# Optimization experiments

Measured on AMD Instinct MI355X. Metric: run time of the kernel, lower is better.

## Reference

```python
import jax, jax.numpy as jnp
import numpy as np

DEP_NUM, HEAD_NUM, BSZ, DIM, REL = 96, 96, 16, 512, 128


def setup_inputs() -> dict:
    key = jax.random.key(0)
    k1, k2, k3, k4 = jax.random.split(key, 4)
    outs = jax.random.normal(k1, (DEP_NUM, BSZ, DIM), dtype=jnp.float32)
    graph_state = jax.random.normal(k2, (HEAD_NUM, BSZ, DIM), dtype=jnp.float32)
    # nn.init.normal_(std=0.02) for both weights, zero biases
    Wt = 0.02 * jax.random.normal(k3, (DIM, 2 * DIM), dtype=jnp.float32)
    bt = jnp.zeros((DIM,), dtype=jnp.float32)
    Wp = 0.02 * jax.random.normal(k4, (REL, DIM), dtype=jnp.float32)
    bp = jnp.zeros((REL,), dtype=jnp.float32)
    return {"outs": outs, "graph_state": graph_state, "Wt": Wt, "bt": bt, "Wp": Wp, "bp": bp}


def reference(outs, graph_state, Wt, bt, Wp, bp):
    # outs: [dep, b, D], graph_state: [head, b, D]
    # Linear(cat(dep, head)) == dep @ Wt[:, :D].T + head @ Wt[:, D:].T + bt
    D = outs.shape[-1]
    dep_proj = jnp.einsum('dbi,ei->dbe', outs, Wt[:, :D])           # [dep, b, D]
    head_proj = jnp.einsum('hbi,ei->hbe', graph_state, Wt[:, D:])   # [head, b, D]
    # broadcast-sum to pairwise: [dep, b, head, D]
    h = jax.nn.relu(dep_proj[:, :, None, :] + jnp.swapaxes(head_proj, 0, 1)[None] + bt)
    # dropout: identity in eval mode
    scores = jnp.einsum('dbhe,re->dbhr', h, Wp) + bp                # [dep, b, head, REL]
    nil = jnp.zeros(scores.shape[:-1] + (1,), dtype=scores.dtype)
    scores = jnp.concatenate([nil, scores], axis=-1)                # [dep, b, head, REL+1]
    return jax.nn.log_softmax(scores, axis=-1)
```

## Files before the change

### kernel.cpp

```cpp
#include <hip/hip_runtime.h>
#include <hip/hip_bf16.h>
#include <math.h>

#define DEP   96
#define HEADS 96
#define BSZ   16
#define DIM   512
#define REL   128
#define RELP  129

typedef __attribute__((ext_vector_type(8))) short short8;
typedef __attribute__((ext_vector_type(4))) float floatx4;

__device__ __forceinline__ unsigned short f2bf(float x) {
    union { float f; unsigned int u; } c; c.f = x;
    unsigned int r = c.u + 0x7fffu + ((c.u >> 16) & 1u);
    return (unsigned short)(r >> 16);
}
__device__ __forceinline__ float bflo2f(unsigned int u) {
    union { unsigned int u; float f; } c; c.u = u << 16; return c.f;
}
__device__ __forceinline__ float bfhi2f(unsigned int u) {
    union { unsigned int u; float f; } c; c.u = u & 0xffff0000u; return c.f;
}

__global__ __launch_bounds__(256) void cvt_kernel(
    const float* __restrict__ Wt, const float* __restrict__ Wp,
    unsigned short* __restrict__ WtB, unsigned short* __restrict__ WpB)
{
    const int chunk = blockIdx.x * 256 + threadIdx.x;
    const float* src; unsigned short* dst; int c;
    if (chunk < 65536) { src = Wt; dst = WtB; c = chunk; }
    else               { src = Wp; dst = WpB; c = chunk - 65536; }
    float4 a = *(const float4*)(src + (size_t)c * 8);
    float4 b = *(const float4*)(src + (size_t)c * 8 + 4);
    uint4 o;
    o.x = (unsigned)f2bf(a.x) | ((unsigned)f2bf(a.y) << 16);
    o.y = (unsigned)f2bf(a.z) | ((unsigned)f2bf(a.w) << 16);
    o.z = (unsigned)f2bf(b.x) | ((unsigned)f2bf(b.y) << 16);
    o.w = (unsigned)f2bf(b.z) | ((unsigned)f2bf(b.w) << 16);
    *(uint4*)(dst + (size_t)c * 8) = o;
}

#define PSS 72

__global__ __launch_bounds__(256) void proj_kernel(
    const float* __restrict__ outs, const float* __restrict__ graph,
    const unsigned short* __restrict__ WtB, const float* __restrict__ bt,
    float* __restrict__ P1, unsigned short* __restrict__ P2B)
{
    const int z = blockIdx.z;
    const float* A = z ? graph : outs;
    const int off  = z ? DIM : 0;
    const int row0 = blockIdx.y * 64;
    const int col0 = blockIdx.x * 64;

    __shared__ unsigned short As[64 * PSS];
    __shared__ unsigned short Ws[64 * PSS];

    const int tid  = threadIdx.x;
    const int lane = tid & 63;
    const int wv   = tid >> 6;
    const int ln15 = lane & 15;
    const int quad = lane >> 4;

    floatx4 acc[4];
    #pragma unroll
    for (int nt = 0; nt < 4; ++nt) acc[nt] = (floatx4){0.f,0.f,0.f,0.f};

    for (int kt = 0; kt < DIM; kt += 64) {
        #pragma unroll
        for (int q = 0; q < 4; ++q) {
            const int slot = q*256 + tid;
            const int r  = slot >> 4;
            const int e4 = (slot & 15) * 4;
            float4 v = *(const float4*)(A + (size_t)(row0 + r) * DIM + kt + e4);
            ushort4 o;
            o.x = f2bf(v.x); o.y = f2bf(v.y); o.z = f2bf(v.z); o.w = f2bf(v.w);
            *(ushort4*)&As[r * PSS + e4] = o;
        }
        #pragma unroll
        for (int q = 0; q < 2; ++q) {
            const int slot = q*256 + tid;
            const int r  = slot >> 3;
            const int e8 = (slot & 7) * 8;
            *(uint4*)&Ws[r * PSS + e8] =
                *(const uint4*)(WtB + (size_t)(col0 + r) * (2*DIM) + off + kt + e8);
        }
        __syncthreads();
        #pragma unroll
        for (int ks = 0; ks < 64; ks += 32) {
            short8 af = *(const short8*)&As[(wv*16 + ln15) * PSS + ks + quad*8];
            #pragma unroll
            for (int nt = 0; nt < 4; ++nt) {
                short8 bf8 = *(const short8*)&Ws[(nt*16 + ln15) * PSS + ks + quad*8];
                acc[nt] = __builtin_amdgcn_mfma_f32_16x16x32_bf16(af, bf8, acc[nt], 0, 0, 0);
            }
        }
        __syncthreads();
    }

    #pragma unroll
    for (int nt = 0; nt < 4; ++nt) {
        #pragma unroll
        for (int reg = 0; reg < 4; ++reg) {
            const int m = row0 + wv*16 + quad*4 + reg;
            const int n = col0 + nt*16 + ln15;
            float v = acc[nt][reg];
            if (!z) P1[(size_t)m * DIM + n] = v + bt[n];
            else    P2B[(size_t)m * DIM + n] = f2bf(v);
        }
    }
}

#define HSS 72
#define WSS 72

__global__ __launch_bounds__(256, 4) void fused_kernel(
    const float* __restrict__ P1, const unsigned short* __restrict__ P2B,
    const unsigned short* __restrict__ WpB, const float* __restrict__ bp,
    float* __restrict__ out)
{
    const int db = blockIdx.x;
    const int b  = db & 15;

    __shared__ float          drow[DIM];
    __shared__ unsigned short hs[96 * HSS];
    __shared__ unsigned short ws[128 * WSS];
    __shared__ float          pmx[96][2];
    __shared__ float          pl [96][2];

    const int tid  = threadIdx.x;
    const int lane = tid & 63;
    const int wv   = tid >> 6;
    const int ln15 = lane & 15;
    const int quad = lane >> 4;
    const int mh   = wv & 1;
    const int nh   = wv >> 1;

    drow[tid]       = P1[(size_t)db * DIM + tid];
    drow[tid + 256] = P1[(size_t)db * DIM + tid + 256];
    __syncthreads();

    floatx4 acc[3][4];
    #pragma unroll
    for (int i = 0; i < 3; ++i)
        #pragma unroll
        for (int j = 0; j < 4; ++j) acc[i][j] = (floatx4){0.f,0.f,0.f,0.f};

    for (int kt = 0; kt < DIM; kt += 64) {
        #pragma unroll
        for (int q = 0; q < 3; ++q) {
            const int slot = q*256 + tid;
            const int h  = slot >> 3;
            const int e8 = (slot & 7) * 8;
            uint4 pv = *(const uint4*)(P2B + ((size_t)h * BSZ + b) * DIM + kt + e8);
            float4 d0 = *(const float4*)&drow[kt + e8];
            float4 d1 = *(const float4*)&drow[kt + e8 + 4];
            float s0 = fmaxf(bflo2f(pv.x) + d0.x, 0.f);
            float s1 = fmaxf(bfhi2f(pv.x) + d0.y, 0.f);
            float s2 = fmaxf(bflo2f(pv.y) + d0.z, 0.f);
            float s3 = fmaxf(bfhi2f(pv.y) + d0.w, 0.f);
            float s4 = fmaxf(bflo2f(pv.z) + d1.x, 0.f);
            float s5 = fmaxf(bfhi2f(pv.z) + d1.y, 0.f);
            float s6 = fmaxf(bflo2f(pv.w) + d1.z, 0.f);
            float s7 = fmaxf(bfhi2f(pv.w) + d1.w, 0.f);
            uint4 o;
            o.x = (unsigned)f2bf(s0) | ((unsigned)f2bf(s1) << 16);
            o.y = (unsigned)f2bf(s2) | ((unsigned)f2bf(s3) << 16);
            o.z = (unsigned)f2bf(s4) | ((unsigned)f2bf(s5) << 16);
            o.w = (unsigned)f2bf(s6) | ((unsigned)f2bf(s7) << 16);
            *(uint4*)&hs[h * HSS + e8] = o;
        }
        #pragma unroll
        for (int q = 0; q < 4; ++q) {
            const int slot = q*256 + tid;
            const int r = slot >> 3;
            const int g = (slot & 7) * 8;
            *(uint4*)&ws[r * WSS + g] =
                *(const uint4*)(WpB + (size_t)r * DIM + kt + g);
        }
        __syncthreads();

        #pragma unroll
        for (int ks = 0; ks < 64; ks += 32) {
            short8 af[3], bf8[4];
            #pragma unroll
            for (int mt = 0; mt < 3; ++mt)
                af[mt] = *(const short8*)&hs[(mh*48 + mt*16 + ln15) * HSS + ks + quad*8];
            #pragma unroll
            for (int nt = 0; nt < 4; ++nt)
                bf8[nt] = *(const short8*)&ws[(nh*64 + nt*16 + ln15) * WSS + ks + quad*8];
            #pragma unroll
            for (int nt = 0; nt < 4; ++nt)
                #pragma unroll
                for (int mt = 0; mt < 3; ++mt)
                    acc[mt][nt] = __builtin_amdgcn_mfma_f32_16x16x32_bf16(
                        af[mt], bf8[nt], acc[mt][nt], 0, 0, 0);
        }
        __syncthreads();
    }

    float bpv[4];
    #pragma unroll
    for (int nt = 0; nt < 4; ++nt) bpv[nt] = bp[nh*64 + nt*16 + ln15];

    #pragma unroll
    for (int mt = 0; mt < 3; ++mt) {
        #pragma unroll
        for (int reg = 0; reg < 4; ++reg) {
            const int m = mh*48 + mt*16 + quad*4 + reg;
            float s[4];
            float mx = -1e30f;
            #pragma unroll
            for (int nt = 0; nt < 4; ++nt) {
                s[nt] = acc[mt][nt][reg] + bpv[nt];
                mx = fmaxf(mx, s[nt]);
            }
            #pragma unroll
            for (int msk = 1; msk < 16; msk <<= 1) mx = fmaxf(mx, __shfl_xor(mx, msk));
            float l = 0.f;
            #pragma unroll
            for (int nt = 0; nt < 4; ++nt) l += __expf(s[nt] - mx);
            #pragma unroll
            for (int msk = 1; msk < 16; msk <<= 1) l += __shfl_xor(l, msk);
            if (ln15 == 0) { pmx[m][nh] = mx; pl[m][nh] = l; }
        }
    }
    __syncthreads();

    #pragma unroll
    for (int mt = 0; mt < 3; ++mt) {
        #pragma unroll
        for (int reg = 0; reg < 4; ++reg) {
            const int m = mh*48 + mt*16 + quad*4 + reg;
            const float mx0 = pmx[m][0], mx1 = pmx[m][1];
            const float l0  = pl[m][0],  l1  = pl[m][1];
            const float MX = fmaxf(fmaxf(mx0, mx1), 0.f);
            const float L  = l0 * __expf(mx0 - MX) + l1 * __expf(mx1 - MX)
                           + __expf(-MX);
            const float lse = MX + __logf(L);

            const size_t base = ((size_t)db * HEADS + m) * RELP;
            #pragma unroll
            for (int nt = 0; nt < 4; ++nt)
                out[base + 1 + nh*64 + nt*16 + ln15] = acc[mt][nt][reg] + bpv[nt] - lse;
            if (nh == 0 && ln15 == 0) out[base] = -lse;
        }
    }
}

extern "C" void kernel_launch(void* const* d_in, const int* in_sizes, int n_in,
                              void* d_out, int out_size, void* d_ws, size_t ws_size,
                              hipStream_t stream) {
    const float* outs  = (const float*)d_in[0];
    const float* graph = (const float*)d_in[1];
    const float* Wt    = (const float*)d_in[2];
    const float* bt    = (const float*)d_in[3];
    const float* Wp    = (const float*)d_in[4];
    const float* bp    = (const float*)d_in[5];
    float* out = (float*)d_out;

    float* P1           = (float*)d_ws;
    unsigned short* P2B = (unsigned short*)(P1 + 786432);
    unsigned short* WpB = P2B + 786432;
    unsigned short* WtB = WpB + 65536;

    cvt_kernel<<<288, 256, 0, stream>>>(Wt, Wp, WtB, WpB);
    proj_kernel<<<dim3(DIM/64, (DEP*BSZ)/64, 2), 256, 0, stream>>>(
        outs, graph, WtB, bt, P1, P2B);
    fused_kernel<<<DEP*BSZ, 256, 0, stream>>>(P1, P2B, WpB, bp, out);
}
```

Baseline: 161.0 us.

## Switch fused pairwise stage to fp16 with packed math and direct global MFMA operand loads

The head projection, the dep row and Wp now use fp16 instead of bf16. The relu(dep+head) combine is done with packed v_pk_add_f16/v_pk_max_f16 directly in registers. The shared-memory staging of the hidden tile and Wp, along with its barriers, is removed, so MFMA operands are loaded straight from global memory (relying on L1/L2 reuse) into f16 MFMAs. This drops LDS traffic, sync and scalar fp32 conversions. The risks are more global/L2 loads per wave, a lower occupancy hint (3 instead of 4 waves per SIMD), and fp16 range and precision in the add.

```diff
diff --git a/kernel.cpp b/kernel.cpp
--- a/kernel.cpp
+++ b/kernel.cpp
@@ -9,37 +9,53 @@
 #define REL   128
 #define RELP  129
 
-typedef __attribute__((ext_vector_type(8))) short short8;
-typedef __attribute__((ext_vector_type(4))) float floatx4;
+typedef __attribute__((ext_vector_type(8))) short     short8;
+typedef __attribute__((ext_vector_type(8))) _Float16  half8;
+typedef __attribute__((ext_vector_type(4))) float     floatx4;
 
 __device__ __forceinline__ unsigned short f2bf(float x) {
     union { float f; unsigned int u; } c; c.f = x;
     unsigned int r = c.u + 0x7fffu + ((c.u >> 16) & 1u);
     return (unsigned short)(r >> 16);
 }
-__device__ __forceinline__ float bflo2f(unsigned int u) {
-    union { unsigned int u; float f; } c; c.u = u << 16; return c.f;
-}
-__device__ __forceinline__ float bfhi2f(unsigned int u) {
-    union { unsigned int u; float f; } c; c.u = u & 0xffff0000u; return c.f;
+__device__ __forceinline__ unsigned short f2h(float x) {
+    union { _Float16 h; unsigned short u; } c;
+    c.h = (_Float16)x;
+    return c.u;
+}
+__device__ __forceinline__ unsigned pk_add_h2(unsigned a, unsigned b) {
+    unsigned r; asm("v_pk_add_f16 %0, %1, %2" : "=v"(r) : "v"(a), "v"(b)); return r;
+}
+__device__ __forceinline__ unsigned pk_max_h2(unsigned a, unsigned b) {
+    unsigned r; asm("v_pk_max_f16 %0, %1, %2" : "=v"(r) : "v"(a), "v"(b)); return r;
 }
 
 __global__ __launch_bounds__(256) void cvt_kernel(
     const float* __restrict__ Wt, const float* __restrict__ Wp,
-    unsigned short* __restrict__ WtB, unsigned short* __restrict__ WpB)
+    unsigned short* __restrict__ WtB, unsigned short* __restrict__ WpH)
 {
     const int chunk = blockIdx.x * 256 + threadIdx.x;
-    const float* src; unsigned short* dst; int c;
-    if (chunk < 65536) { src = Wt; dst = WtB; c = chunk; }
-    else               { src = Wp; dst = WpB; c = chunk - 65536; }
-    float4 a = *(const float4*)(src + (size_t)c * 8);
-    float4 b = *(const float4*)(src + (size_t)c * 8 + 4);
-    uint4 o;
-    o.x = (unsigned)f2bf(a.x) | ((unsigned)f2bf(a.y) << 16);
-    o.y = (unsigned)f2bf(a.z) | ((unsigned)f2bf(a.w) << 16);
-    o.z = (unsigned)f2bf(b.x) | ((unsigned)f2bf(b.y) << 16);
-    o.w = (unsigned)f2bf(b.z) | ((unsigned)f2bf(b.w) << 16);
-    *(uint4*)(dst + (size_t)c * 8) = o;
+    if (chunk < 65536) {
+        const int c = chunk;
+        float4 a = *(const float4*)(Wt + (size_t)c * 8);
+        float4 b = *(const float4*)(Wt + (size_t)c * 8 + 4);
+        uint4 o;
+        o.x = (unsigned)f2bf(a.x) | ((unsigned)f2bf(a.y) << 16);
+        o.y = (unsigned)f2bf(a.z) | ((unsigned)f2bf(a.w) << 16);
+        o.z = (unsigned)f2bf(b.x) | ((unsigned)f2bf(b.y) << 16);
+        o.w = (unsigned)f2bf(b.z) | ((unsigned)f2bf(b.w) << 16);
+        *(uint4*)(WtB + (size_t)c * 8) = o;
+    } else {
+        const int c = chunk - 65536;
+        float4 a = *(const float4*)(Wp + (size_t)c * 8);
+        float4 b = *(const float4*)(Wp + (size_t)c * 8 + 4);
+        uint4 o;
+        o.x = (unsigned)f2h(a.x) | ((unsigned)f2h(a.y) << 16);
+        o.y = (unsigned)f2h(a.z) | ((unsigned)f2h(a.w) << 16);
+        o.z = (unsigned)f2h(b.x) | ((unsigned)f2h(b.y) << 16);
+        o.w = (unsigned)f2h(b.z) | ((unsigned)f2h(b.w) << 16);
+        *(uint4*)(WpH + (size_t)c * 8) = o;
+    }
 }
 
 #define PSS 72
@@ -47,7 +63,7 @@
 __global__ __launch_bounds__(256) void proj_kernel(
     const float* __restrict__ outs, const float* __restrict__ graph,
     const unsigned short* __restrict__ WtB, const float* __restrict__ bt,
-    float* __restrict__ P1, unsigned short* __restrict__ P2B)
+    float* __restrict__ P1, unsigned short* __restrict__ P2H)
 {
     const int z = blockIdx.z;
     const float* A = z ? graph : outs;
@@ -108,27 +124,22 @@
             const int n = col0 + nt*16 + ln15;
             float v = acc[nt][reg];
             if (!z) P1[(size_t)m * DIM + n] = v + bt[n];
-            else    P2B[(size_t)m * DIM + n] = f2bf(v);
-        }
-    }
-}
-
-#define HSS 72
-#define WSS 72
-
-__global__ __launch_bounds__(256, 4) void fused_kernel(
-    const float* __restrict__ P1, const unsigned short* __restrict__ P2B,
-    const unsigned short* __restrict__ WpB, const float* __restrict__ bp,
+            else    P2H[(size_t)m * DIM + n] = f2h(v);
+        }
+    }
+}
+
+__global__ __launch_bounds__(256, 3) void fused_kernel(
+    const float* __restrict__ P1, const unsigned short* __restrict__ P2H,
+    const unsigned short* __restrict__ WpH, const float* __restrict__ bp,
     float* __restrict__ out)
 {
     const int db = blockIdx.x;
     const int b  = db & 15;
 
-    __shared__ float          drow[DIM];
-    __shared__ unsigned short hs[96 * HSS];
-    __shared__ unsigned short ws[128 * WSS];
-    __shared__ float          pmx[96][2];
-    __shared__ float          pl [96][2];
+    __shared__ unsigned short drowH[DIM];
+    __shared__ float pmx[96][2];
+    __shared__ float pl [96][2];
 
     const int tid  = threadIdx.x;
     const int lane = tid & 63;
@@ -138,67 +149,51 @@
     const int mh   = wv & 1;
     const int nh   = wv >> 1;
 
-    drow[tid]       = P1[(size_t)db * DIM + tid];
-    drow[tid + 256] = P1[(size_t)db * DIM + tid + 256];
+    {
+        float2 v = *(const float2*)(P1 + (size_t)db * DIM + tid*2);
+        drowH[tid*2]   = f2h(v.x);
+        drowH[tid*2+1] = f2h(v.y);
+    }
     __syncthreads();
 
+    const unsigned short* pA[3];
+    #pragma unroll
+    for (int mt = 0; mt < 3; ++mt)
+        pA[mt] = P2H + ((size_t)(mh*48 + mt*16 + ln15) * BSZ + b) * DIM + quad*8;
+    const unsigned short* pB[4];
+    #pragma unroll
+    for (int nt = 0; nt < 4; ++nt)
+        pB[nt] = WpH + (size_t)(nh*64 + nt*16 + ln15) * DIM + quad*8;
+
     floatx4 acc[3][4];
     #pragma unroll
     for (int i = 0; i < 3; ++i)
         #pragma unroll
         for (int j = 0; j < 4; ++j) acc[i][j] = (floatx4){0.f,0.f,0.f,0.f};
 
-    for (int kt = 0; kt < DIM; kt += 64) {
-        #pragma unroll
-        for (int q = 0; q < 3; ++q) {
-            const int slot = q*256 + tid;
-            const int h  = slot >> 3;
-            const int e8 = (slot & 7) * 8;
-            uint4 pv = *(const uint4*)(P2B + ((size_t)h * BSZ + b) * DIM + kt + e8);
-            float4 d0 = *(const float4*)&drow[kt + e8];
-            float4 d1 = *(const float4*)&drow[kt + e8 + 4];
-            float s0 = fmaxf(bflo2f(pv.x) + d0.x, 0.f);
-            float s1 = fmaxf(bfhi2f(pv.x) + d0.y, 0.f);
-            float s2 = fmaxf(bflo2f(pv.y) + d0.z, 0.f);
-            float s3 = fmaxf(bfhi2f(pv.y) + d0.w, 0.f);
-            float s4 = fmaxf(bflo2f(pv.z) + d1.x, 0.f);
-            float s5 = fmaxf(bfhi2f(pv.z) + d1.y, 0.f);
-            float s6 = fmaxf(bflo2f(pv.w) + d1.z, 0.f);
-            float s7 = fmaxf(bfhi2f(pv.w) + d1.w, 0.f);
-            uint4 o;
-            o.x = (unsigned)f2bf(s0) | ((unsigned)f2bf(s1) << 16);
-            o.y = (unsigned)f2bf(s2) | ((unsigned)f2bf(s3) << 16);
-            o.z = (unsigned)f2bf(s4) | ((unsigned)f2bf(s5) << 16);
-            o.w = (unsigned)f2bf(s6) | ((unsigned)f2bf(s7) << 16);
-            *(uint4*)&hs[h * HSS + e8] = o;
-        }
-        #pragma unroll
-        for (int q = 0; q < 4; ++q) {
-            const int slot = q*256 + tid;
-            const int r = slot >> 3;
-            const int g = (slot & 7) * 8;
-            *(uint4*)&ws[r * WSS + g] =
-                *(const uint4*)(WpB + (size_t)r * DIM + kt + g);
-        }
-        __syncthreads();
-
-        #pragma unroll
-        for (int ks = 0; ks < 64; ks += 32) {
-            short8 af[3], bf8[4];
+    #pragma unroll 4
+    for (int kk = 0; kk < DIM; kk += 32) {
+        uint4 dv = *(const uint4*)&drowH[kk + quad*8];
+
+        union { uint4 u; half8 h; } af[3], bf[4];
+        #pragma unroll
+        for (int mt = 0; mt < 3; ++mt) {
+            uint4 pv = *(const uint4*)(pA[mt] + kk);
+            af[mt].u.x = pk_max_h2(pk_add_h2(pv.x, dv.x), 0u);
+            af[mt].u.y = pk_max_h2(pk_add_h2(pv.y, dv.y), 0u);
+            af[mt].u.z = pk_max_h2(pk_add_h2(pv.z, dv.z), 0u);
+            af[mt].u.w = pk_max_h2(pk_add_h2(pv.w, dv.w), 0u);
+        }
+        #pragma unroll
+        for (int nt = 0; nt < 4; ++nt)
+            bf[nt].u = *(const uint4*)(pB[nt] + kk);
+
+        #pragma unroll
+        for (int nt = 0; nt < 4; ++nt)
             #pragma unroll
             for (int mt = 0; mt < 3; ++mt)
-                af[mt] = *(const short8*)&hs[(mh*48 + mt*16 + ln15) * HSS + ks + quad*8];
-            #pragma unroll
-            for (int nt = 0; nt < 4; ++nt)
-                bf8[nt] = *(const short8*)&ws[(nh*64 + nt*16 + ln15) * WSS + ks + quad*8];
-            #pragma unroll
-            for (int nt = 0; nt < 4; ++nt)
-                #pragma unroll
-                for (int mt = 0; mt < 3; ++mt)
-                    acc[mt][nt] = __builtin_amdgcn_mfma_f32_16x16x32_bf16(
-                        af[mt], bf8[nt], acc[mt][nt], 0, 0, 0);
-        }
-        __syncthreads();
+                acc[mt][nt] = __builtin_amdgcn_mfma_f32_16x16x32_f16(
+                    af[mt].h, bf[nt].h, acc[mt][nt], 0, 0, 0);
     }
 
     float bpv[4];
@@ -262,12 +257,12 @@
     float* out = (float*)d_out;
 
     float* P1           = (float*)d_ws;
-    unsigned short* P2B = (unsigned short*)(P1 + 786432);
-    unsigned short* WpB = P2B + 786432;
-    unsigned short* WtB = WpB + 65536;
-
-    cvt_kernel<<<288, 256, 0, stream>>>(Wt, Wp, WtB, WpB);
+    unsigned short* P2H = (unsigned short*)(P1 + 786432);
+    unsigned short* WpH = P2H + 786432;
+    unsigned short* WtB = WpH + 65536;
+
+    cvt_kernel<<<288, 256, 0, stream>>>(Wt, Wp, WtB, WpH);
     proj_kernel<<<dim3(DIM/64, (DEP*BSZ)/64, 2), 256, 0, stream>>>(
-        outs, graph, WtB, bt, P1, P2B);
-    fused_kernel<<<DEP*BSZ, 256, 0, stream>>>(P1, P2B, WpB, bp, out);
-}
+        outs, graph, WtB, bt, P1, P2H);
+    fused_kernel<<<DEP*BSZ, 256, 0, stream>>>(P1, P2H, WpH, bp, out);
+}
```

New measurement: 205.2 us. 1.27x slower.
